# Optimization experiments

Hardware: AMD Instinct MI355X
Metric: run time of the kernel (lower is better)

The kernel has to match this reference:

```python
import jax, jax.numpy as jnp
from jax import lax
import numpy as np

B, S, D = 4096, 5, 64
HS = 1024 - 64 + 1  # 961-tap kernel -> output length D + HS - 1 = 1024
VSA = D + HS - 1    # 1024
LN_EPS = 1e-3       # keras LayerNormalization default epsilon


def setup_inputs() -> dict:
    key = jax.random.key(0)
    k1, k2, k3 = jax.random.split(key, 3)
    values = jax.random.normal(k1, (B, S, D), dtype=jnp.float32)
    h = jax.random.normal(k2, (S, HS), dtype=jnp.float32) * 0.05  # random_normal init
    symbols = jax.random.normal(k3, (S, D), dtype=jnp.float32)    # stddev=1.0 init
    gamma = jnp.ones((VSA,), dtype=jnp.float32)
    beta = jnp.zeros((VSA,), dtype=jnp.float32)
    return {"values": values, "h": h, "symbols": symbols, "gamma": gamma, "beta": beta}


def _small_conv_net(x, h, gamma, beta):
    """ConvLayerWithLearnableH + silu + LayerNorm (dropout omitted: stochastic).

    x: [B, S, D]; each seq position i is cross-correlated (tf.nn.conv1d does
    no kernel flip) with its own kernel h[i] after padding (HS-1) both sides,
    giving output length D + HS - 1. Vectorized as a grouped 1D conv with
    feature_group_count = S (seq positions act as channels).
    """
    hs = h.shape[1]
    y = lax.conv_general_dilated(
        x,                      # [B, S(=C), D(=W)]
        h[:, None, :],          # [S(=O), 1(=I/groups), hs(=W)]
        window_strides=(1,),
        padding=[(hs - 1, hs - 1)],
        dimension_numbers=("NCW", "OIW", "NCW"),
        feature_group_count=x.shape[1],
    )                           # [B, S, D + hs - 1]
    y = jax.nn.silu(y)
    mu = jnp.mean(y, axis=-1, keepdims=True)
    var = jnp.var(y, axis=-1, keepdims=True)
    return (y - mu) * lax.rsqrt(var + LN_EPS) * gamma + beta


def reference(values, h, symbols, gamma, beta):
    # values_projected / symbol_projected: [B, S, VSA]
    vp = _small_conv_net(values, h, gamma, beta)
    sp = _small_conv_net(jnp.broadcast_to(symbols[None, :, :], values.shape), h, gamma, beta)
    # sign-based cosine similarity: S[b, j, i] = mean_d sign(vp[b,i,d]) * sign(vp[b,i,d] + sp[b,j,d])
    xi = vp[:, None, :, :]   # [B, 1, S, VSA]  (X_i_expanded)
    xj = sp[:, :, None, :]   # [B, S, 1, VSA]  (X_j_expanded from C)
    scores = jnp.mean(jnp.sign(xi) * jnp.sign(xi + xj), axis=-1)  # [B, S, S]
    scores = jax.nn.softmax(scores, axis=-1)
    att = jnp.einsum("bji,bid->bjd", scores, vp)  # [B, S, VSA]
    return jax.nn.silu(att * sp)
```

## Files before the change

### kernel.cpp

```cpp
#include <hip/hip_runtime.h>
#include <math.h>

#define BB   4096
#define SS   5
#define DD   64
#define HSZ  961
#define VSA  1024
#define NT   256
#define NB   2
#define LNE  1e-3f

#define POFF 64
#define PW   1092

typedef float v4f __attribute__((ext_vector_type(4)));

__device__ __forceinline__ float silu_f(float x) { return x / (1.f + __expf(-x)); }

template <int CTRL>
__device__ __forceinline__ float dpp_add(float x) {
    int t = __builtin_amdgcn_update_dpp(0, __builtin_bit_cast(int, x),
                                        CTRL, 0xf, 0xf, false);
    return x + __builtin_bit_cast(float, t);
}
__device__ __forceinline__ float wave64_sum_l63(float x) {
    x = dpp_add<0x111>(x);
    x = dpp_add<0x112>(x);
    x = dpp_add<0x114>(x);
    x = dpp_add<0x118>(x);
    x = dpp_add<0x142>(x);
    x = dpp_add<0x143>(x);
    return x;
}

__global__ __launch_bounds__(NT)
void sp_kernel(const float* __restrict__ symbols, const float* __restrict__ h,
               const float* __restrict__ gamma, const float* __restrict__ beta,
               float* __restrict__ sp, float* __restrict__ hpadG)
{
    __shared__ float hpad[PW];
    __shared__ float red[4][2];
    const int s = blockIdx.x;
    const int tid = threadIdx.x;
    const int lane = tid & 63, wave = tid >> 6;

    for (int r = tid; r < PW; r += NT) {
        const float v = (r >= POFF && r <= POFF + 960) ? h[s * HSZ + (r - POFF)] : 0.f;
        hpad[r] = v;
        hpadG[s * PW + r] = v;
    }
    __syncthreads();

    const int base = 1020 - 4 * tid;
    float hw[8];
    *(float4*)&hw[0] = *(const float4*)&hpad[base];
    float acc[4] = {0.f, 0.f, 0.f, 0.f};
    const float* xp = symbols + s * DD;
#pragma unroll
    for (int c = 0; c < 16; c++) {
        *(float4*)&hw[4] = *(const float4*)&hpad[base + 4 * (c + 1)];
        const float x0 = xp[4 * c + 0];
        const float x1 = xp[4 * c + 1];
        const float x2 = xp[4 * c + 2];
        const float x3 = xp[4 * c + 3];
        acc[0] += x0 * hw[4]; acc[0] += x1 * hw[5]; acc[0] += x2 * hw[6]; acc[0] += x3 * hw[7];
        acc[1] += x0 * hw[3]; acc[1] += x1 * hw[4]; acc[1] += x2 * hw[5]; acc[1] += x3 * hw[6];
        acc[2] += x0 * hw[2]; acc[2] += x1 * hw[3]; acc[2] += x2 * hw[4]; acc[2] += x3 * hw[5];
        acc[3] += x0 * hw[1]; acc[3] += x1 * hw[2]; acc[3] += x2 * hw[3]; acc[3] += x3 * hw[4];
        hw[0] = hw[4]; hw[1] = hw[5]; hw[2] = hw[6]; hw[3] = hw[7];
    }

    float ys[4];
    float lsum = 0.f, lsq = 0.f;
#pragma unroll
    for (int j = 0; j < 4; j++) {
        ys[j] = silu_f(acc[j]);
        lsum += ys[j]; lsq += ys[j] * ys[j];
    }
    lsum = wave64_sum_l63(lsum);
    lsq  = wave64_sum_l63(lsq);
    if (lane == 63) { red[wave][0] = lsum; red[wave][1] = lsq; }
    __syncthreads();
    float s0 = 0.f, s1 = 0.f;
#pragma unroll
    for (int w = 0; w < 4; w++) { s0 += red[w][0]; s1 += red[w][1]; }
    const float mean = s0 * (1.f / VSA);
    const float rstd = rsqrtf(s1 * (1.f / VSA) - mean * mean + LNE);

    const float4 g4 = *(const float4*)&gamma[4 * tid];
    const float4 b4 = *(const float4*)&beta[4 * tid];
    float4 o;
    o.x = (ys[0] - mean) * rstd * g4.x + b4.x;
    o.y = (ys[1] - mean) * rstd * g4.y + b4.y;
    o.z = (ys[2] - mean) * rstd * g4.z + b4.z;
    o.w = (ys[3] - mean) * rstd * g4.w + b4.w;
    *(float4*)&sp[s * VSA + 4 * tid] = o;
}

__global__ __launch_bounds__(NT, 2)
void main_kernel(const float* __restrict__ values, const float* __restrict__ hpadG,
                 const float* __restrict__ sp, const float* __restrict__ gamma,
                 const float* __restrict__ beta, float* __restrict__ out)
{
    __shared__ __align__(16) float hs[SS * PW];
    __shared__ __align__(16) float xs[NB][SS][DD];
    __shared__ float red[SS][NB][4][2];
    __shared__ int   scorered[NB][4][SS * SS];
    __shared__ float wbuf[NB][SS * SS];

    const int tid = threadIdx.x;
    const int lane = tid & 63, wave = tid >> 6;
    const int b0 = blockIdx.x * NB;
    const int base = 1020 - 4 * tid;

    for (int i = tid; i < (SS * PW) / 4; i += NT)
        ((float4*)hs)[i] = ((const float4*)hpadG)[i];

    if (tid < (NB * SS * DD) / 4) {
        ((float4*)xs)[tid] =
            ((const float4*)(values + (size_t)b0 * (SS * DD)))[tid];
    }
    __syncthreads();

    float vp[NB][SS][4];

#pragma unroll
    for (int s = 0; s < SS; s++) {
        const float* hp = hs + s * PW + base;
        float hw[8];
        *(float4*)&hw[0] = *(const float4*)hp;
        float acc[NB][4];
#pragma unroll
        for (int nb = 0; nb < NB; nb++)
            acc[nb][0] = acc[nb][1] = acc[nb][2] = acc[nb][3] = 0.f;
#pragma unroll 1
        for (int c = 0; c < 16; c++) {
            *(float4*)&hw[4] = *(const float4*)(hp + 4 * c + 4);
#pragma unroll
            for (int nb = 0; nb < NB; nb++) {
                const float4 xv = *(const float4*)&xs[nb][s][4 * c];
                acc[nb][0] += xv.x * hw[4]; acc[nb][0] += xv.y * hw[5]; acc[nb][0] += xv.z * hw[6]; acc[nb][0] += xv.w * hw[7];
                acc[nb][1] += xv.x * hw[3]; acc[nb][1] += xv.y * hw[4]; acc[nb][1] += xv.z * hw[5]; acc[nb][1] += xv.w * hw[6];
                acc[nb][2] += xv.x * hw[2]; acc[nb][2] += xv.y * hw[3]; acc[nb][2] += xv.z * hw[4]; acc[nb][2] += xv.w * hw[5];
                acc[nb][3] += xv.x * hw[1]; acc[nb][3] += xv.y * hw[2]; acc[nb][3] += xv.z * hw[3]; acc[nb][3] += xv.w * hw[4];
            }
            hw[0] = hw[4]; hw[1] = hw[5]; hw[2] = hw[6]; hw[3] = hw[7];
        }
        __builtin_amdgcn_sched_barrier(0);
#pragma unroll
        for (int nb = 0; nb < NB; nb++) {
            float lsum = 0.f, lsq = 0.f;
#pragma unroll
            for (int j = 0; j < 4; j++) {
                const float y = silu_f(acc[nb][j]);
                vp[nb][s][j] = y; lsum += y; lsq += y * y;
            }
            lsum = wave64_sum_l63(lsum);
            lsq  = wave64_sum_l63(lsq);
            if (lane == 63) { red[s][nb][wave][0] = lsum; red[s][nb][wave][1] = lsq; }
        }
        __builtin_amdgcn_sched_barrier(0);
    }
    __syncthreads();

    const float4 g4 = *(const float4*)&gamma[4 * tid];
    const float4 b4 = *(const float4*)&beta[4 * tid];
#pragma unroll
    for (int s = 0; s < SS; s++) {
#pragma unroll
        for (int nb = 0; nb < NB; nb++) {
            float s0 = 0.f, s1 = 0.f;
#pragma unroll
            for (int w = 0; w < 4; w++) { s0 += red[s][nb][w][0]; s1 += red[s][nb][w][1]; }
            const float mean = s0 * (1.f / VSA);
            const float rstd = rsqrtf(s1 * (1.f / VSA) - mean * mean + LNE);
            vp[nb][s][0] = (vp[nb][s][0] - mean) * rstd * g4.x + b4.x;
            vp[nb][s][1] = (vp[nb][s][1] - mean) * rstd * g4.y + b4.y;
            vp[nb][s][2] = (vp[nb][s][2] - mean) * rstd * g4.z + b4.z;
            vp[nb][s][3] = (vp[nb][s][3] - mean) * rstd * g4.w + b4.w;
        }
    }

    float sp4[SS][4];
#pragma unroll
    for (int i = 0; i < SS; i++)
        *(float4*)&sp4[i][0] = *(const float4*)&sp[i * VSA + 4 * tid];

#pragma unroll
    for (int nb = 0; nb < NB; nb++) {
        int neq[SS * SS];
#pragma unroll
        for (int p = 0; p < SS * SS; p++) neq[p] = 0;
#pragma unroll
        for (int jj = 0; jj < 4; jj++) {
            unsigned long long bvi[SS];
#pragma unroll
            for (int i = 0; i < SS; i++) bvi[i] = __ballot(vp[nb][i][jj] > 0.f);
#pragma unroll
            for (int j = 0; j < SS; j++) {
                const float sjv = sp4[j][jj];
#pragma unroll
                for (int i = 0; i < SS; i++) {
                    const unsigned long long bs = __ballot(vp[nb][i][jj] + sjv > 0.f);
                    neq[j * SS + i] += (int)__popcll(bvi[i] ^ bs);
                }
            }
        }
        if (lane == 0) {
#pragma unroll
            for (int p = 0; p < SS * SS; p++) scorered[nb][wave][p] = neq[p];
        }
    }
    __syncthreads();

    if (tid < NB * SS) {
        const int nb = tid / SS, j = tid - nb * SS;
        float sc[SS];
#pragma unroll
        for (int i = 0; i < SS; i++) {
            const int nq = scorered[nb][0][j * SS + i] + scorered[nb][1][j * SS + i]
                         + scorered[nb][2][j * SS + i] + scorered[nb][3][j * SS + i];
            sc[i] = 1.f - (2.f / VSA) * (float)nq;
        }
        float m = sc[0];
#pragma unroll
        for (int i = 1; i < SS; i++) m = fmaxf(m, sc[i]);
        float e[SS], ssum = 0.f;
#pragma unroll
        for (int i = 0; i < SS; i++) { e[i] = __expf(sc[i] - m); ssum += e[i]; }
        const float inv = 1.f / ssum;
#pragma unroll
        for (int i = 0; i < SS; i++) wbuf[nb][j * SS + i] = e[i] * inv;
    }
    __syncthreads();

#pragma unroll
    for (int nb = 0; nb < NB; nb++) {
        const size_t obase = (size_t)(b0 + nb) * SS * VSA + 4 * tid;
#pragma unroll
        for (int j = 0; j < SS; j++) {
            float wj[SS];
#pragma unroll
            for (int i = 0; i < SS; i++) wj[i] = wbuf[nb][j * SS + i];
            float att[4] = {0.f, 0.f, 0.f, 0.f};
#pragma unroll
            for (int i = 0; i < SS; i++) {
                const float wi = wj[i];
#pragma unroll
                for (int e = 0; e < 4; e++) att[e] += wi * vp[nb][i][e];
            }
            v4f o;
            o.x = silu_f(att[0] * sp4[j][0]);
            o.y = silu_f(att[1] * sp4[j][1]);
            o.z = silu_f(att[2] * sp4[j][2]);
            o.w = silu_f(att[3] * sp4[j][3]);
            __builtin_nontemporal_store(o, (v4f*)&out[obase + (size_t)j * VSA]);
        }
    }
}

extern "C" void kernel_launch(void* const* d_in, const int* in_sizes, int n_in,
                              void* d_out, int out_size, void* d_ws, size_t ws_size,
                              hipStream_t stream) {
    const float* values  = (const float*)d_in[0];
    const float* h       = (const float*)d_in[1];
    const float* symbols = (const float*)d_in[2];
    const float* gamma   = (const float*)d_in[3];
    const float* beta    = (const float*)d_in[4];
    float* out   = (float*)d_out;
    float* sp    = (float*)d_ws;
    float* hpadG = (float*)d_ws + SS * VSA;

    sp_kernel<<<SS, NT, 0, stream>>>(symbols, h, gamma, beta, sp, hpadG);
    main_kernel<<<BB / NB, NT, 0, stream>>>(values, hpadG, sp, gamma, beta, out);
}
```

Before: 187.9 us.

## Interleave batch pair in LDS and use packed v2f FMAs for convolution

Stores the two batch rows interleaved in shared memory so each tap's x values for both batches form a float2. The inner convolution then uses packed two-wide FMAs (v_pk_fma_f32 on CDNA) with the filter tap broadcast, which halves the FMA instruction count. The loop is also fully unrolled, with the next filter and x values loaded ahead of each step to hide LDS latency. In exchange the values load becomes scalar strided reads instead of float4 copies, and register use rises, which may hurt occupancy.

```diff
diff --git a/kernel.cpp b/kernel.cpp
--- a/kernel.cpp
+++ b/kernel.cpp
@@ -14,8 +14,10 @@
 #define PW   1092
 
 typedef float v4f __attribute__((ext_vector_type(4)));
+typedef float v2f __attribute__((ext_vector_type(2)));
 
 __device__ __forceinline__ float silu_f(float x) { return x / (1.f + __expf(-x)); }
+__device__ __forceinline__ v2f splat2(float x) { v2f r; r.x = x; r.y = x; return r; }
 
 template <int CTRL>
 __device__ __forceinline__ float dpp_add(float x) {
@@ -103,7 +105,7 @@
                  const float* __restrict__ beta, float* __restrict__ out)
 {
     __shared__ __align__(16) float hs[SS * PW];
-    __shared__ __align__(16) float xs[NB][SS][DD];
+    __shared__ __align__(16) float xsI[SS][DD][NB];
     __shared__ float red[SS][NB][4][2];
     __shared__ int   scorered[NB][4][SS * SS];
     __shared__ float wbuf[NB][SS * SS];
@@ -116,9 +118,11 @@
     for (int i = tid; i < (SS * PW) / 4; i += NT)
         ((float4*)hs)[i] = ((const float4*)hpadG)[i];
 
-    if (tid < (NB * SS * DD) / 4) {
-        ((float4*)xs)[tid] =
-            ((const float4*)(values + (size_t)b0 * (SS * DD)))[tid];
+    for (int i = tid; i < SS * DD; i += NT) {
+        v2f v;
+        v.x = values[(size_t)(b0 + 0) * (SS * DD) + i];
+        v.y = values[(size_t)(b0 + 1) * (SS * DD) + i];
+        ((v2f*)xsI)[i] = v;
     }
     __syncthreads();
 
@@ -127,24 +131,39 @@
 #pragma unroll
     for (int s = 0; s < SS; s++) {
         const float* hp = hs + s * PW + base;
-        float hw[8];
-        *(float4*)&hw[0] = *(const float4*)hp;
-        float acc[NB][4];
-#pragma unroll
-        for (int nb = 0; nb < NB; nb++)
-            acc[nb][0] = acc[nb][1] = acc[nb][2] = acc[nb][3] = 0.f;
-#pragma unroll 1
+        const v2f* xp = (const v2f*)&xsI[s][0][0];
+        float4 hLo = *(const float4*)hp;
+        float4 hHi = *(const float4*)(hp + 4);
+        v2f x0 = xp[0], x1 = xp[1], x2 = xp[2], x3 = xp[3];
+        v2f acc2[4] = {};
+#pragma unroll
         for (int c = 0; c < 16; c++) {
-            *(float4*)&hw[4] = *(const float4*)(hp + 4 * c + 4);
-#pragma unroll
-            for (int nb = 0; nb < NB; nb++) {
-                const float4 xv = *(const float4*)&xs[nb][s][4 * c];
-                acc[nb][0] += xv.x * hw[4]; acc[nb][0] += xv.y * hw[5]; acc[nb][0] += xv.z * hw[6]; acc[nb][0] += xv.w * hw[7];
-                acc[nb][1] += xv.x * hw[3]; acc[nb][1] += xv.y * hw[4]; acc[nb][1] += xv.z * hw[5]; acc[nb][1] += xv.w * hw[6];
-                acc[nb][2] += xv.x * hw[2]; acc[nb][2] += xv.y * hw[3]; acc[nb][2] += xv.z * hw[4]; acc[nb][2] += xv.w * hw[5];
-                acc[nb][3] += xv.x * hw[1]; acc[nb][3] += xv.y * hw[2]; acc[nb][3] += xv.z * hw[3]; acc[nb][3] += xv.w * hw[4];
-            }
-            hw[0] = hw[4]; hw[1] = hw[5]; hw[2] = hw[6]; hw[3] = hw[7];
+            float4 hNx = {};
+            v2f n0 = {}, n1 = {}, n2 = {}, n3 = {};
+            if (c < 15) {
+                hNx = *(const float4*)(hp + 4 * c + 8);
+                n0 = xp[4 * c + 4]; n1 = xp[4 * c + 5];
+                n2 = xp[4 * c + 6]; n3 = xp[4 * c + 7];
+            }
+            acc2[0] = __builtin_elementwise_fma(x0, splat2(hHi.x), acc2[0]);
+            acc2[0] = __builtin_elementwise_fma(x1, splat2(hHi.y), acc2[0]);
+            acc2[0] = __builtin_elementwise_fma(x2, splat2(hHi.z), acc2[0]);
+            acc2[0] = __builtin_elementwise_fma(x3, splat2(hHi.w), acc2[0]);
+            acc2[1] = __builtin_elementwise_fma(x0, splat2(hLo.w), acc2[1]);
+            acc2[1] = __builtin_elementwise_fma(x1, splat2(hHi.x), acc2[1]);
+            acc2[1] = __builtin_elementwise_fma(x2, splat2(hHi.y), acc2[1]);
+            acc2[1] = __builtin_elementwise_fma(x3, splat2(hHi.z), acc2[1]);
+            acc2[2] = __builtin_elementwise_fma(x0, splat2(hLo.z), acc2[2]);
+            acc2[2] = __builtin_elementwise_fma(x1, splat2(hLo.w), acc2[2]);
+            acc2[2] = __builtin_elementwise_fma(x2, splat2(hHi.x), acc2[2]);
+            acc2[2] = __builtin_elementwise_fma(x3, splat2(hHi.y), acc2[2]);
+            acc2[3] = __builtin_elementwise_fma(x0, splat2(hLo.y), acc2[3]);
+            acc2[3] = __builtin_elementwise_fma(x1, splat2(hLo.z), acc2[3]);
+            acc2[3] = __builtin_elementwise_fma(x2, splat2(hLo.w), acc2[3]);
+            acc2[3] = __builtin_elementwise_fma(x3, splat2(hHi.x), acc2[3]);
+            __builtin_amdgcn_sched_barrier(0);
+            hLo = hHi; hHi = hNx;
+            x0 = n0; x1 = n1; x2 = n2; x3 = n3;
         }
         __builtin_amdgcn_sched_barrier(0);
 #pragma unroll
@@ -152,7 +171,7 @@
             float lsum = 0.f, lsq = 0.f;
 #pragma unroll
             for (int j = 0; j < 4; j++) {
-                const float y = silu_f(acc[nb][j]);
+                const float y = silu_f(acc2[j][nb]);
                 vp[nb][s][j] = y; lsum += y; lsq += y * y;
             }
             lsum = wave64_sum_l63(lsum);
```

Result: faster. 169.7 us (-9.7%).
